# Optimization experiments

Hardware: AMD Instinct MI355X
Metric: run time of the kernel (lower is better)

Reference implementation:

```python
import jax, jax.numpy as jnp
import numpy as np

K_STEPS = 12      # number_of_prediction_steps
TEMP = 0.1        # temperature
EPS = 1e-12       # F.normalize eps


def setup_inputs() -> dict:
    key = jax.random.key(0)
    ks = jax.random.split(key, 8)
    B, T, W, D, C = 128, 512, 64, 128, 256
    g = lambda k, shape, s: (jax.random.normal(k, shape, jnp.float32) * s)
    return {
        "rr_windows": jax.random.normal(ks[0], (B, T, W), jnp.float32),
        # Encoder: Linear(window_size -> latent_dim)
        "We": g(ks[1], (W, D), 0.1), "be": jnp.zeros((D,), jnp.float32),
        # ARBlock: single-layer GRU(latent_dim -> context_dim)
        "Wi": g(ks[2], (D, 3 * C), 0.1), "Wh": g(ks[3], (C, 3 * C), 0.1),
        "bi": jnp.zeros((3 * C,), jnp.float32), "bh": jnp.zeros((3 * C,), jnp.float32),
        # Wk: K_STEPS Linears(context_dim -> latent_dim), stacked
        "Wk_w": g(ks[4], (K_STEPS, C, D), 0.1), "Wk_b": jnp.zeros((K_STEPS, D), jnp.float32),
    }


def _l2norm(x):
    n = jnp.linalg.norm(x, axis=-1, keepdims=True)
    return x / jnp.maximum(n, EPS)


def _gru(z_seq, Wi, Wh, bi, bh):
    # z_seq: [B, T, D] -> contexts [B, T, C]
    B = z_seq.shape[0]
    C = Wh.shape[0]
    x_proj = z_seq @ Wi + bi                       # [B, T, 3C] (precompute input gates)

    def step(h, x):
        hg = h @ Wh + bh
        xr, xz, xn = jnp.split(x, 3, axis=-1)
        hr, hz, hn = jnp.split(hg, 3, axis=-1)
        r = jax.nn.sigmoid(xr + hr)
        z = jax.nn.sigmoid(xz + hz)
        n = jnp.tanh(xn + r * hn)
        h_new = (1.0 - z) * n + z * h
        return h_new, h_new

    h0 = jnp.zeros((B, C), z_seq.dtype)
    _, hs = jax.lax.scan(step, h0, jnp.swapaxes(x_proj, 0, 1))  # [T, B, C]
    return jnp.swapaxes(hs, 0, 1)


def reference(rr_windows, We, be, Wi, Wh, bi, bh, Wk_w, Wk_b):
    B, T, W = rr_windows.shape
    # Encoder + normalize
    z_seq = _l2norm(rr_windows @ We + be)          # [B, T, D]
    # AR context
    c_seq = _gru(z_seq, Wi, Wh, bi, bh)            # [B, T, C]

    Tp = T - K_STEPS
    c_t = c_seq[:, :Tp, :]                         # [B, Tp, C]
    # all K predictions at once, then normalize
    pred = jnp.einsum('btc,kcd->kbtd', c_t, Wk_w) + Wk_b[:, None, None, :]
    pred = _l2norm(pred)                           # [K, B, Tp, D]
    # z_future[k, :, t] = z_seq[:, t + k + 1]
    zf = jnp.stack([jax.lax.dynamic_slice_in_dim(z_seq, k + 1, Tp, axis=1)
                    for k in range(K_STEPS)])      # [K, B, Tp, D]
    # logits[k, t, i, j] = pred[k, i, t] . z_future[k, j, t] / temp
    logits = jnp.einsum('kbtd,kctd->ktbc', pred, zf) / TEMP  # [K, Tp, B, B]

    lse = jax.nn.logsumexp(logits, axis=-1)        # [K, Tp, B]
    diag = jnp.einsum('ktbb->ktb', logits)
    avg_loss = jnp.mean(lse - diag)
    labels = jnp.arange(B)
    avg_accuracy = jnp.mean((jnp.argmax(logits, axis=-1) == labels).astype(jnp.float32)) * 100.0
    return avg_loss, avg_accuracy, z_seq, c_seq
```

## Files before the change

kernel.cpp:

```cpp
#include <hip/hip_runtime.h>
#include <math.h>

#define B_  128
#define T_  512
#define W_  64
#define D_  128
#define C_  256
#define K_  12
#define TP_ 500
#define N_SAMPLES 768000

typedef _Float16 half2v __attribute__((ext_vector_type(2)));
typedef _Float16 f16x8  __attribute__((ext_vector_type(8)));
typedef float    f32x4  __attribute__((ext_vector_type(4)));

__device__ __forceinline__ unsigned int pack2(float a, float b) {
  unsigned short ua = __builtin_bit_cast(unsigned short, (_Float16)a);
  unsigned short ub = __builtin_bit_cast(unsigned short, (_Float16)b);
  return (unsigned int)ua | ((unsigned int)ub << 16);
}

__global__ __launch_bounds__(128) void z_kernel(const float* __restrict__ rr,
                                                const float* __restrict__ We,
                                                const float* __restrict__ be,
                                                float* __restrict__ z_out,
                                                _Float16* __restrict__ z16) {
  int row = blockIdx.x;
  int d   = threadIdx.x;
  __shared__ float s_rr[64];
  __shared__ float s_red[128];
  if (d < 64) s_rr[d] = rr[row * 64 + d];
  __syncthreads();
  float acc = be[d];
#pragma unroll
  for (int w = 0; w < 64; ++w) acc = fmaf(s_rr[w], We[w * 128 + d], acc);
  s_red[d] = acc * acc;
  __syncthreads();
#pragma unroll
  for (int s = 64; s > 0; s >>= 1) {
    if (d < s) s_red[d] += s_red[d + s];
    __syncthreads();
  }
  float inv = 1.0f / fmaxf(sqrtf(s_red[0]), 1e-12f);
  float zv = acc * inv;
  z_out[row * 128 + d] = zv;
  z16[(size_t)row * 128 + d] = (_Float16)zv;
}

__global__ __launch_bounds__(256) void wiT_kernel(const float* __restrict__ Wi,
                                                  _Float16* __restrict__ wiT) {
  int id = blockIdx.x * 256 + threadIdx.x;
  int k   = id / 768;
  int col = id % 768;
  wiT[(size_t)col * 128 + k] = (_Float16)Wi[id];
}

__global__ __launch_bounds__(256, 2) void xproj_mfma(const _Float16* __restrict__ z16,
                                                     const _Float16* __restrict__ wiT,
                                                     const float* __restrict__ bi,
                                                     _Float16* __restrict__ xp) {
  int rb  = blockIdx.x * 128;
  int cb  = blockIdx.y * 128;
  int tid  = threadIdx.x;
  int wv   = tid >> 6;
  int lane = tid & 63;
  int n15  = lane & 15;
  int q    = lane >> 4;

  __shared__ __align__(16) _Float16 sA[128 * 72];
  __shared__ __align__(16) _Float16 sB[128 * 72];

  f32x4 acc[2][8];
#pragma unroll
  for (int a = 0; a < 2; ++a)
#pragma unroll
    for (int m = 0; m < 8; ++m) acc[a][m] = (f32x4){0.f, 0.f, 0.f, 0.f};

#pragma unroll
  for (int p = 0; p < 2; ++p) {
#pragma unroll
    for (int it = 0; it < 4; ++it) {
      int id = tid + it * 256;
      int r  = id >> 3;
      int c8 = (id & 7) * 8;
      *(uint4*)(&sA[r * 72 + c8]) =
          *(const uint4*)(z16 + (size_t)(rb + r) * 128 + p * 64 + c8);
      *(uint4*)(&sB[r * 72 + c8]) =
          *(const uint4*)(wiT + (size_t)(cb + r) * 128 + p * 64 + c8);
    }
    __syncthreads();
#pragma unroll
    for (int ks = 0; ks < 2; ++ks) {
      f16x8 bf[2];
#pragma unroll
      for (int ntl = 0; ntl < 2; ++ntl)
        bf[ntl] = *(const f16x8*)(&sB[((wv * 2 + ntl) * 16 + n15) * 72 + ks * 32 + q * 8]);
#pragma unroll
      for (int mt = 0; mt < 8; ++mt) {
        f16x8 af = *(const f16x8*)(&sA[(mt * 16 + n15) * 72 + ks * 32 + q * 8]);
        acc[0][mt] = __builtin_amdgcn_mfma_f32_16x16x32_f16(af, bf[0], acc[0][mt], 0, 0, 0);
        acc[1][mt] = __builtin_amdgcn_mfma_f32_16x16x32_f16(af, bf[1], acc[1][mt], 0, 0, 0);
      }
    }
    __syncthreads();
  }

#pragma unroll
  for (int ntl = 0; ntl < 2; ++ntl) {
    int col = cb + (wv * 2 + ntl) * 16 + n15;
    float bb = bi[col];
#pragma unroll
    for (int mt = 0; mt < 8; ++mt) {
#pragma unroll
      for (int r = 0; r < 4; ++r) {
        int row = rb + mt * 16 + q * 4 + r;
        xp[(size_t)row * 768 + col] = (_Float16)(acc[ntl][mt][r] + bb);
      }
    }
  }
}

__global__ __launch_bounds__(256) void whT_kernel(const float* __restrict__ Wh,
                                                  unsigned int* __restrict__ whT) {
  int g = blockIdx.x * 256 + threadIdx.x;
  int i = g / 768;
  int j = g % 768;
  float lo = Wh[(size_t)(2 * i) * 768 + j];
  float hi = Wh[(size_t)(2 * i + 1) * 768 + j];
  whT[(size_t)j * 128 + i] = pack2(lo, hi);
}

__global__ __launch_bounds__(256) void wkT_kernel(const float* __restrict__ Wk_w,
                                                  _Float16* __restrict__ wkT) {
  int id = blockIdx.x * 256 + threadIdx.x;
  int k = id >> 15;
  int rem = id & 32767;
  int c = rem >> 7;
  int d = rem & 127;
  wkT[((size_t)k * 128 + d) * 256 + c] = (_Float16)Wk_w[id];
}

__global__ __launch_bounds__(1024) void gru_kernel(const _Float16* __restrict__ xp,
                                                   const unsigned int* __restrict__ whT,
                                                   const float* __restrict__ bh,
                                                   float* __restrict__ c_out,
                                                   _Float16* __restrict__ c16) {
  __shared__ __align__(16) unsigned int s_h2[2][128];
  int tid  = threadIdx.x;
  int b    = blockIdx.x;
  int w    = tid >> 6;
  int lane = tid & 63;
  int n15  = lane & 15;
  int q    = lane >> 4;
  int ch   = w * 16 + n15;

  uint4 wf[3][8];
#pragma unroll
  for (int g = 0; g < 3; ++g) {
    const uint4* src = (const uint4*)(whT + (size_t)(g * 256 + ch) * 128);
#pragma unroll
    for (int kt = 0; kt < 8; ++kt) wf[g][kt] = src[kt * 4 + q];
  }

  if (tid < 128) s_h2[0][tid] = 0u;

  float bhr = bh[ch], bhz = bh[256 + ch], bhn = bh[512 + ch];
  const _Float16* xb = xp + (size_t)b * 512 * 768;
  float xr_n = (float)xb[ch];
  float xz_n = (float)xb[256 + ch];
  float xn_n = (float)xb[512 + ch];
  float h = 0.f;
  __syncthreads();

  for (int t = 0; t < 512; ++t) {
    const char* hb = (const char*)(&s_h2[t & 1][0]) + q * 16;
    f32x4 a0 = (f32x4){0.f, 0.f, 0.f, 0.f};
    f32x4 a1 = (f32x4){0.f, 0.f, 0.f, 0.f};
    f32x4 a2 = (f32x4){0.f, 0.f, 0.f, 0.f};
#pragma unroll
    for (int kt = 0; kt < 8; ++kt) {
      f16x8 af = *(const f16x8*)(hb + kt * 64);
      a0 = __builtin_amdgcn_mfma_f32_16x16x32_f16(af, __builtin_bit_cast(f16x8, wf[0][kt]), a0, 0, 0, 0);
      a1 = __builtin_amdgcn_mfma_f32_16x16x32_f16(af, __builtin_bit_cast(f16x8, wf[1][kt]), a1, 0, 0, 0);
      a2 = __builtin_amdgcn_mfma_f32_16x16x32_f16(af, __builtin_bit_cast(f16x8, wf[2][kt]), a2, 0, 0, 0);
    }

    float xr_c = xr_n, xz_c = xz_n, xn_c = xn_n;
    if (t < 511) {
      const _Float16* p = xb + (size_t)(t + 1) * 768;
      xr_n = (float)p[ch];
      xz_n = (float)p[256 + ch];
      xn_n = (float)p[512 + ch];
    }

    float hr = a0[0] + bhr;
    float hz = a1[0] + bhz;
    float hn = a2[0] + bhn;
    float r = __builtin_amdgcn_rcpf(1.f + __expf(-(xr_c + hr)));
    float z = __builtin_amdgcn_rcpf(1.f + __expf(-(xz_c + hz)));
    float y = xn_c + r * hn;
    y = fminf(10.f, fmaxf(-10.f, y));
    float ey = __expf(-2.f * y);
    float n = (1.f - ey) * __builtin_amdgcn_rcpf(1.f + ey);
    h = (1.f - z) * n + z * h;

    if (q == 0) {
      ((_Float16*)(&s_h2[(t & 1) ^ 1][0]))[ch] = (_Float16)h;
      c_out[((size_t)b * 512 + t) * 256 + ch] = h;
      c16[((size_t)b * 512 + t) * 256 + ch] = (_Float16)h;
    }
    __syncthreads();
  }
}

__global__ __launch_bounds__(256, 2) void cpc_kernel(const _Float16* __restrict__ z16,
                                                     const _Float16* __restrict__ c16,
                                                     const _Float16* __restrict__ wkT,
                                                     const float* __restrict__ Wk_b,
                                                     float2* __restrict__ partials) {
  int k   = blockIdx.x;
  int t   = blockIdx.y;
  int tid = threadIdx.x;
  int wv   = tid >> 6;
  int lane = tid & 63;
  int n15  = lane & 15;
  int q    = lane >> 4;

  __shared__ __align__(16) _Float16 sA[128 * 72];
  __shared__ __align__(16) _Float16 sB[128 * 72];
  __shared__ __align__(16) _Float16 sP[128 * 136];
  __shared__ float s_bias[128];

  if (tid < 128) s_bias[tid] = Wk_b[k * 128 + tid];

  f32x4 acc[2][8];
#pragma unroll
  for (int a = 0; a < 2; ++a)
#pragma unroll
    for (int m = 0; m < 8; ++m) acc[a][m] = (f32x4){0.f, 0.f, 0.f, 0.f};

  const _Float16* wk_base = wkT + (size_t)k * 128 * 256;

  for (int p = 0; p < 4; ++p) {
#pragma unroll
    for (int it = 0; it < 4; ++it) {
      int id = tid + it * 256;
      int r  = id >> 3;
      int c8 = (id & 7) * 8;
      *(uint4*)(&sA[r * 72 + c8]) =
          *(const uint4*)(wk_base + (size_t)r * 256 + p * 64 + c8);
      *(uint4*)(&sB[r * 72 + c8]) =
          *(const uint4*)(c16 + ((size_t)r * 512 + t) * 256 + p * 64 + c8);
    }
    __syncthreads();
#pragma unroll
    for (int ks = 0; ks < 2; ++ks) {
      f16x8 bf[2];
#pragma unroll
      for (int ntl = 0; ntl < 2; ++ntl)
        bf[ntl] = *(const f16x8*)(&sB[((wv * 2 + ntl) * 16 + n15) * 72 + ks * 32 + q * 8]);
#pragma unroll
      for (int mt = 0; mt < 8; ++mt) {
        f16x8 af = *(const f16x8*)(&sA[(mt * 16 + n15) * 72 + ks * 32 + q * 8]);
        acc[0][mt] = __builtin_amdgcn_mfma_f32_16x16x32_f16(af, bf[0], acc[0][mt], 0, 0, 0);
        acc[1][mt] = __builtin_amdgcn_mfma_f32_16x16x32_f16(af, bf[1], acc[1][mt], 0, 0, 0);
      }
    }
    __syncthreads();
  }

  float scale[2];
#pragma unroll
  for (int ntl = 0; ntl < 2; ++ntl) {
    float ssq = 0.f;
#pragma unroll
    for (int mt = 0; mt < 8; ++mt)
#pragma unroll
      for (int r = 0; r < 4; ++r) {
        float v = acc[ntl][mt][r] + s_bias[mt * 16 + q * 4 + r];
        acc[ntl][mt][r] = v;
        ssq = fmaf(v, v, ssq);
      }
    ssq += __shfl_xor(ssq, 16);
    ssq += __shfl_xor(ssq, 32);
    scale[ntl] = 10.0f / fmaxf(sqrtf(ssq), 1e-12f);
  }

#pragma unroll
  for (int ntl = 0; ntl < 2; ++ntl) {
    int bi = (wv * 2 + ntl) * 16 + n15;
#pragma unroll
    for (int mt = 0; mt < 8; ++mt) {
      uint2 v;
      v.x = pack2(acc[ntl][mt][0] * scale[ntl], acc[ntl][mt][1] * scale[ntl]);
      v.y = pack2(acc[ntl][mt][2] * scale[ntl], acc[ntl][mt][3] * scale[ntl]);
      *(uint2*)(&sP[bi * 136 + mt * 16 + q * 4]) = v;
    }
  }

  int tz = t + k + 1;
#pragma unroll
  for (int it = 0; it < 4; ++it) {
    int id = tid + it * 256;
    int r  = id >> 3;
    int d8 = (id & 7) * 8;
    *(uint4*)(&sA[r * 72 + d8]) =
        *(const uint4*)(z16 + ((size_t)r * 512 + tz) * 128 + d8);
    *(uint4*)(&sB[r * 72 + d8]) =
        *(const uint4*)(z16 + ((size_t)r * 512 + tz) * 128 + 64 + d8);
  }
  __syncthreads();

  f32x4 lacc[2][8];
#pragma unroll
  for (int a = 0; a < 2; ++a)
#pragma unroll
    for (int m = 0; m < 8; ++m) lacc[a][m] = (f32x4){0.f, 0.f, 0.f, 0.f};

#pragma unroll
  for (int pan = 0; pan < 2; ++pan) {
#pragma unroll
    for (int ks = 0; ks < 2; ++ks) {
      f16x8 af[2];
#pragma unroll
      for (int mtl = 0; mtl < 2; ++mtl)
        af[mtl] = *(const f16x8*)(&sP[((wv * 2 + mtl) * 16 + n15) * 136 + pan * 64 + ks * 32 + q * 8]);
#pragma unroll
      for (int nt = 0; nt < 8; ++nt) {
        f16x8 bf = pan
          ? *(const f16x8*)(&sB[(nt * 16 + n15) * 72 + ks * 32 + q * 8])
          : *(const f16x8*)(&sA[(nt * 16 + n15) * 72 + ks * 32 + q * 8]);
        lacc[0][nt] = __builtin_amdgcn_mfma_f32_16x16x32_f16(af[0], bf, lacc[0][nt], 0, 0, 0);
        lacc[1][nt] = __builtin_amdgcn_mfma_f32_16x16x32_f16(af[1], bf, lacc[1][nt], 0, 0, 0);
      }
    }
  }

  float loss_acc = 0.f, corr_acc = 0.f;
#pragma unroll
  for (int mtl = 0; mtl < 2; ++mtl) {
    int dnt = wv * 2 + mtl;
#pragma unroll
    for (int r = 0; r < 4; ++r) {
      int b = (wv * 2 + mtl) * 16 + q * 4 + r;
      float m = -1e30f; int idx = 1 << 30; float diag = 0.f;
#pragma unroll
      for (int nt = 0; nt < 8; ++nt) {
        float v = lacc[mtl][nt][r];
        int c2 = nt * 16 + n15;
        if (v > m) { m = v; idx = c2; }
        if (nt == dnt && n15 == (b & 15)) diag = v;
      }
#pragma unroll
      for (int s = 1; s <= 8; s <<= 1) {
        float om = __shfl_xor(m, s);
        int   oi = __shfl_xor(idx, s);
        if (om > m || (om == m && oi < idx)) { m = om; idx = oi; }
      }
      float e = 0.f;
#pragma unroll
      for (int nt = 0; nt < 8; ++nt) e += __expf(lacc[mtl][nt][r] - m);
#pragma unroll
      for (int s = 1; s <= 8; s <<= 1) e += __shfl_xor(e, s);
      if (n15 == (b & 15)) {
        float lse = m + __logf(e);
        loss_acc += lse - diag;
        corr_acc += (idx == b) ? 1.0f : 0.0f;
      }
    }
  }
#pragma unroll
  for (int s = 1; s <= 32; s <<= 1) {
    loss_acc += __shfl_xor(loss_acc, s);
    corr_acc += __shfl_xor(corr_acc, s);
  }

  if (lane == 0) {
    s_bias[wv * 2 + 0] = loss_acc;
    s_bias[wv * 2 + 1] = corr_acc;
  }
  __syncthreads();
  if (tid == 0) {
    float L = s_bias[0] + s_bias[2] + s_bias[4] + s_bias[6];
    float C = s_bias[1] + s_bias[3] + s_bias[5] + s_bias[7];
    partials[k * TP_ + t] = make_float2(L, C);
  }
}

__global__ __launch_bounds__(256) void reduce_kernel(const float2* __restrict__ partials,
                                                     float* __restrict__ out) {
  float l = 0.f, c = 0.f;
  for (int i = threadIdx.x; i < K_ * TP_; i += 256) {
    float2 v = partials[i];
    l += v.x; c += v.y;
  }
#pragma unroll
  for (int s = 1; s <= 32; s <<= 1) {
    l += __shfl_xor(l, s);
    c += __shfl_xor(c, s);
  }
  __shared__ float sl[4], sc[4];
  int wv = threadIdx.x >> 6;
  if ((threadIdx.x & 63) == 0) { sl[wv] = l; sc[wv] = c; }
  __syncthreads();
  if (threadIdx.x == 0) {
    float L = sl[0] + sl[1] + sl[2] + sl[3];
    float C = sc[0] + sc[1] + sc[2] + sc[3];
    out[0] = L * (float)(1.0 / (double)N_SAMPLES);
    out[1] = C * (float)(100.0 / (double)N_SAMPLES);
  }
}

extern "C" void kernel_launch(void* const* d_in, const int* in_sizes, int n_in,
                              void* d_out, int out_size, void* d_ws, size_t ws_size,
                              hipStream_t stream) {
  (void)in_sizes; (void)n_in; (void)out_size; (void)ws_size;
  const float* rr  = (const float*)d_in[0];
  const float* We  = (const float*)d_in[1];
  const float* be  = (const float*)d_in[2];
  const float* Wi  = (const float*)d_in[3];
  const float* Wh  = (const float*)d_in[4];
  const float* bi  = (const float*)d_in[5];
  const float* bh  = (const float*)d_in[6];
  const float* Wkw = (const float*)d_in[7];
  const float* Wkb = (const float*)d_in[8];

  float* out = (float*)d_out;
  float* z   = out + 2;
  float* c   = z + (size_t)B_ * T_ * D_;

  char* ws = (char*)d_ws;
  unsigned int* whT   = (unsigned int*)ws;
  _Float16*     wkT16 = (_Float16*)(ws + 393216);
  _Float16*     z16   = (_Float16*)(ws + 1179648);
  _Float16*     c16   = (_Float16*)(ws + 17956864);
  _Float16*     xp    = (_Float16*)(ws + 51511296);
  _Float16*     wiT16 = (_Float16*)(ws + 152174592);
  float2*       parts = (float2*)(ws + 51511296);

  hipMemsetAsync(d_out, 0, 2 * sizeof(float), stream);
  z_kernel<<<B_ * T_, 128, 0, stream>>>(rr, We, be, z, z16);
  wiT_kernel<<<384, 256, 0, stream>>>(Wi, wiT16);
  whT_kernel<<<384, 256, 0, stream>>>(Wh, whT);
  wkT_kernel<<<1536, 256, 0, stream>>>(Wkw, wkT16);
  xproj_mfma<<<dim3(512, 6), 256, 0, stream>>>(z16, wiT16, bi, xp);
  gru_kernel<<<B_, 1024, 0, stream>>>(xp, whT, bh, c, c16);
  cpc_kernel<<<dim3(K_, TP_), 256, 0, stream>>>(z16, c16, wkT16, Wkb, parts);
  reduce_kernel<<<1, 256, 0, stream>>>(parts, out);
}
```

Baseline: 994.7 us.

## Loop all prediction steps inside one CPC block to reuse context tile

The CPC kernel now launches one block per time step and loops over the 12 prediction heads internally. The context tile for that time step is loaded into shared memory once and reused across all heads, instead of being reloaded by 12 separate blocks. In exchange the grid shrinks from 6000 to 500 blocks. Shared memory use also rises, which forces one block per CU and may hurt occupancy and latency hiding. The reduce kernel now sums only 500 partials.

```diff
diff --git a/kernel.cpp b/kernel.cpp
--- a/kernel.cpp
+++ b/kernel.cpp
@@ -213,184 +213,196 @@
   }
 }
 
-__global__ __launch_bounds__(256, 2) void cpc_kernel(const _Float16* __restrict__ z16,
+__global__ __launch_bounds__(256, 1) void cpc_kernel(const _Float16* __restrict__ z16,
                                                      const _Float16* __restrict__ c16,
                                                      const _Float16* __restrict__ wkT,
                                                      const float* __restrict__ Wk_b,
                                                      float2* __restrict__ partials) {
-  int k   = blockIdx.x;
-  int t   = blockIdx.y;
+  int t   = blockIdx.x;
   int tid = threadIdx.x;
   int wv   = tid >> 6;
   int lane = tid & 63;
   int n15  = lane & 15;
   int q    = lane >> 4;
 
-  __shared__ __align__(16) _Float16 sA[128 * 72];
-  __shared__ __align__(16) _Float16 sB[128 * 72];
+  __shared__ __align__(16) _Float16 sCt[4][128 * 72];
+  __shared__ __align__(16) _Float16 sW[2][128 * 72];
   __shared__ __align__(16) _Float16 sP[128 * 136];
-  __shared__ float s_bias[128];
-
-  if (tid < 128) s_bias[tid] = Wk_b[k * 128 + tid];
-
-  f32x4 acc[2][8];
-#pragma unroll
-  for (int a = 0; a < 2; ++a)
-#pragma unroll
-    for (int m = 0; m < 8; ++m) acc[a][m] = (f32x4){0.f, 0.f, 0.f, 0.f};
-
-  const _Float16* wk_base = wkT + (size_t)k * 128 * 256;
-
-  for (int p = 0; p < 4; ++p) {
+  __shared__ float s_biasAll[12 * 128];
+  __shared__ float s_red[8];
+
+#pragma unroll
+  for (int it = 0; it < 16; ++it) {
+    int id  = tid + it * 256;
+    int p   = id >> 10;
+    int rem = id & 1023;
+    int r   = rem >> 3;
+    int c8  = (rem & 7) * 8;
+    *(uint4*)(&sCt[p][r * 72 + c8]) =
+        *(const uint4*)(c16 + ((size_t)r * 512 + t) * 256 + p * 64 + c8);
+  }
+  for (int i = tid; i < 12 * 128; i += 256) s_biasAll[i] = Wk_b[i];
+  __syncthreads();
+
+  float loss_acc = 0.f, corr_acc = 0.f;
+
+  for (int k = 0; k < 12; ++k) {
+    const _Float16* wk_base = wkT + (size_t)k * 128 * 256;
+
+    f32x4 acc[2][8];
+#pragma unroll
+    for (int a = 0; a < 2; ++a)
+#pragma unroll
+      for (int m = 0; m < 8; ++m) acc[a][m] = (f32x4){0.f, 0.f, 0.f, 0.f};
+
+    for (int p = 0; p < 4; ++p) {
+#pragma unroll
+      for (int it = 0; it < 4; ++it) {
+        int id = tid + it * 256;
+        int r  = id >> 3;
+        int c8 = (id & 7) * 8;
+        *(uint4*)(&sW[p & 1][r * 72 + c8]) =
+            *(const uint4*)(wk_base + (size_t)r * 256 + p * 64 + c8);
+      }
+      __syncthreads();
+#pragma unroll
+      for (int ks = 0; ks < 2; ++ks) {
+        f16x8 bf[2];
+#pragma unroll
+        for (int ntl = 0; ntl < 2; ++ntl)
+          bf[ntl] = *(const f16x8*)(&sCt[p][((wv * 2 + ntl) * 16 + n15) * 72 + ks * 32 + q * 8]);
+#pragma unroll
+        for (int mt = 0; mt < 8; ++mt) {
+          f16x8 af = *(const f16x8*)(&sW[p & 1][(mt * 16 + n15) * 72 + ks * 32 + q * 8]);
+          acc[0][mt] = __builtin_amdgcn_mfma_f32_16x16x32_f16(af, bf[0], acc[0][mt], 0, 0, 0);
+          acc[1][mt] = __builtin_amdgcn_mfma_f32_16x16x32_f16(af, bf[1], acc[1][mt], 0, 0, 0);
+        }
+      }
+      __syncthreads();
+    }
+
+    const float* s_bias = s_biasAll + k * 128;
+    float scale[2];
+#pragma unroll
+    for (int ntl = 0; ntl < 2; ++ntl) {
+      float ssq = 0.f;
+#pragma unroll
+      for (int mt = 0; mt < 8; ++mt)
+#pragma unroll
+        for (int r = 0; r < 4; ++r) {
+          float v = acc[ntl][mt][r] + s_bias[mt * 16 + q * 4 + r];
+          acc[ntl][mt][r] = v;
+          ssq = fmaf(v, v, ssq);
+        }
+      ssq += __shfl_xor(ssq, 16);
+      ssq += __shfl_xor(ssq, 32);
+      scale[ntl] = 10.0f / fmaxf(sqrtf(ssq), 1e-12f);
+    }
+
+#pragma unroll
+    for (int ntl = 0; ntl < 2; ++ntl) {
+      int bi = (wv * 2 + ntl) * 16 + n15;
+#pragma unroll
+      for (int mt = 0; mt < 8; ++mt) {
+        uint2 v;
+        v.x = pack2(acc[ntl][mt][0] * scale[ntl], acc[ntl][mt][1] * scale[ntl]);
+        v.y = pack2(acc[ntl][mt][2] * scale[ntl], acc[ntl][mt][3] * scale[ntl]);
+        *(uint2*)(&sP[bi * 136 + mt * 16 + q * 4]) = v;
+      }
+    }
+
+    int tz = t + k + 1;
 #pragma unroll
     for (int it = 0; it < 4; ++it) {
       int id = tid + it * 256;
       int r  = id >> 3;
-      int c8 = (id & 7) * 8;
-      *(uint4*)(&sA[r * 72 + c8]) =
-          *(const uint4*)(wk_base + (size_t)r * 256 + p * 64 + c8);
-      *(uint4*)(&sB[r * 72 + c8]) =
-          *(const uint4*)(c16 + ((size_t)r * 512 + t) * 256 + p * 64 + c8);
-    }
-    __syncthreads();
-#pragma unroll
-    for (int ks = 0; ks < 2; ++ks) {
-      f16x8 bf[2];
-#pragma unroll
-      for (int ntl = 0; ntl < 2; ++ntl)
-        bf[ntl] = *(const f16x8*)(&sB[((wv * 2 + ntl) * 16 + n15) * 72 + ks * 32 + q * 8]);
-#pragma unroll
-      for (int mt = 0; mt < 8; ++mt) {
-        f16x8 af = *(const f16x8*)(&sA[(mt * 16 + n15) * 72 + ks * 32 + q * 8]);
-        acc[0][mt] = __builtin_amdgcn_mfma_f32_16x16x32_f16(af, bf[0], acc[0][mt], 0, 0, 0);
-        acc[1][mt] = __builtin_amdgcn_mfma_f32_16x16x32_f16(af, bf[1], acc[1][mt], 0, 0, 0);
-      }
-    }
-    __syncthreads();
-  }
-
-  float scale[2];
-#pragma unroll
-  for (int ntl = 0; ntl < 2; ++ntl) {
-    float ssq = 0.f;
-#pragma unroll
-    for (int mt = 0; mt < 8; ++mt)
+      int d8 = (id & 7) * 8;
+      *(uint4*)(&sW[0][r * 72 + d8]) =
+          *(const uint4*)(z16 + ((size_t)r * 512 + tz) * 128 + d8);
+      *(uint4*)(&sW[1][r * 72 + d8]) =
+          *(const uint4*)(z16 + ((size_t)r * 512 + tz) * 128 + 64 + d8);
+    }
+    __syncthreads();
+
+    f32x4 lacc[2][8];
+#pragma unroll
+    for (int a = 0; a < 2; ++a)
+#pragma unroll
+      for (int m = 0; m < 8; ++m) lacc[a][m] = (f32x4){0.f, 0.f, 0.f, 0.f};
+
+#pragma unroll
+    for (int pan = 0; pan < 2; ++pan) {
+#pragma unroll
+      for (int ks = 0; ks < 2; ++ks) {
+        f16x8 af[2];
+#pragma unroll
+        for (int mtl = 0; mtl < 2; ++mtl)
+          af[mtl] = *(const f16x8*)(&sP[((wv * 2 + mtl) * 16 + n15) * 136 + pan * 64 + ks * 32 + q * 8]);
+#pragma unroll
+        for (int nt = 0; nt < 8; ++nt) {
+          f16x8 bf = *(const f16x8*)(&sW[pan][(nt * 16 + n15) * 72 + ks * 32 + q * 8]);
+          lacc[0][nt] = __builtin_amdgcn_mfma_f32_16x16x32_f16(af[0], bf, lacc[0][nt], 0, 0, 0);
+          lacc[1][nt] = __builtin_amdgcn_mfma_f32_16x16x32_f16(af[1], bf, lacc[1][nt], 0, 0, 0);
+        }
+      }
+    }
+
+#pragma unroll
+    for (int mtl = 0; mtl < 2; ++mtl) {
+      int dnt = wv * 2 + mtl;
 #pragma unroll
       for (int r = 0; r < 4; ++r) {
-        float v = acc[ntl][mt][r] + s_bias[mt * 16 + q * 4 + r];
-        acc[ntl][mt][r] = v;
-        ssq = fmaf(v, v, ssq);
-      }
-    ssq += __shfl_xor(ssq, 16);
-    ssq += __shfl_xor(ssq, 32);
-    scale[ntl] = 10.0f / fmaxf(sqrtf(ssq), 1e-12f);
-  }
-
-#pragma unroll
-  for (int ntl = 0; ntl < 2; ++ntl) {
-    int bi = (wv * 2 + ntl) * 16 + n15;
-#pragma unroll
-    for (int mt = 0; mt < 8; ++mt) {
-      uint2 v;
-      v.x = pack2(acc[ntl][mt][0] * scale[ntl], acc[ntl][mt][1] * scale[ntl]);
-      v.y = pack2(acc[ntl][mt][2] * scale[ntl], acc[ntl][mt][3] * scale[ntl]);
-      *(uint2*)(&sP[bi * 136 + mt * 16 + q * 4]) = v;
-    }
-  }
-
-  int tz = t + k + 1;
-#pragma unroll
-  for (int it = 0; it < 4; ++it) {
-    int id = tid + it * 256;
-    int r  = id >> 3;
-    int d8 = (id & 7) * 8;
-    *(uint4*)(&sA[r * 72 + d8]) =
-        *(const uint4*)(z16 + ((size_t)r * 512 + tz) * 128 + d8);
-    *(uint4*)(&sB[r * 72 + d8]) =
-        *(const uint4*)(z16 + ((size_t)r * 512 + tz) * 128 + 64 + d8);
-  }
-  __syncthreads();
-
-  f32x4 lacc[2][8];
-#pragma unroll
-  for (int a = 0; a < 2; ++a)
-#pragma unroll
-    for (int m = 0; m < 8; ++m) lacc[a][m] = (f32x4){0.f, 0.f, 0.f, 0.f};
-
-#pragma unroll
-  for (int pan = 0; pan < 2; ++pan) {
-#pragma unroll
-    for (int ks = 0; ks < 2; ++ks) {
-      f16x8 af[2];
-#pragma unroll
-      for (int mtl = 0; mtl < 2; ++mtl)
-        af[mtl] = *(const f16x8*)(&sP[((wv * 2 + mtl) * 16 + n15) * 136 + pan * 64 + ks * 32 + q * 8]);
-#pragma unroll
-      for (int nt = 0; nt < 8; ++nt) {
-        f16x8 bf = pan
-          ? *(const f16x8*)(&sB[(nt * 16 + n15) * 72 + ks * 32 + q * 8])
-          : *(const f16x8*)(&sA[(nt * 16 + n15) * 72 + ks * 32 + q * 8]);
-        lacc[0][nt] = __builtin_amdgcn_mfma_f32_16x16x32_f16(af[0], bf, lacc[0][nt], 0, 0, 0);
-        lacc[1][nt] = __builtin_amdgcn_mfma_f32_16x16x32_f16(af[1], bf, lacc[1][nt], 0, 0, 0);
-      }
-    }
-  }
-
-  float loss_acc = 0.f, corr_acc = 0.f;
-#pragma unroll
-  for (int mtl = 0; mtl < 2; ++mtl) {
-    int dnt = wv * 2 + mtl;
-#pragma unroll
-    for (int r = 0; r < 4; ++r) {
-      int b = (wv * 2 + mtl) * 16 + q * 4 + r;
-      float m = -1e30f; int idx = 1 << 30; float diag = 0.f;
-#pragma unroll
-      for (int nt = 0; nt < 8; ++nt) {
-        float v = lacc[mtl][nt][r];
-        int c2 = nt * 16 + n15;
-        if (v > m) { m = v; idx = c2; }
-        if (nt == dnt && n15 == (b & 15)) diag = v;
-      }
-#pragma unroll
-      for (int s = 1; s <= 8; s <<= 1) {
-        float om = __shfl_xor(m, s);
-        int   oi = __shfl_xor(idx, s);
-        if (om > m || (om == m && oi < idx)) { m = om; idx = oi; }
-      }
-      float e = 0.f;
-#pragma unroll
-      for (int nt = 0; nt < 8; ++nt) e += __expf(lacc[mtl][nt][r] - m);
-#pragma unroll
-      for (int s = 1; s <= 8; s <<= 1) e += __shfl_xor(e, s);
-      if (n15 == (b & 15)) {
-        float lse = m + __logf(e);
-        loss_acc += lse - diag;
-        corr_acc += (idx == b) ? 1.0f : 0.0f;
-      }
-    }
-  }
+        int b = (wv * 2 + mtl) * 16 + q * 4 + r;
+        float m = -1e30f; int idx = 1 << 30; float diag = 0.f;
+#pragma unroll
+        for (int nt = 0; nt < 8; ++nt) {
+          float v = lacc[mtl][nt][r];
+          int c2 = nt * 16 + n15;
+          if (v > m) { m = v; idx = c2; }
+          if (nt == dnt && n15 == (b & 15)) diag = v;
+        }
+#pragma unroll
+        for (int s = 1; s <= 8; s <<= 1) {
+          float om = __shfl_xor(m, s);
+          int   oi = __shfl_xor(idx, s);
+          if (om > m || (om == m && oi < idx)) { m = om; idx = oi; }
+        }
+        float e = 0.f;
+#pragma unroll
+        for (int nt = 0; nt < 8; ++nt) e += __expf(lacc[mtl][nt][r] - m);
+#pragma unroll
+        for (int s = 1; s <= 8; s <<= 1) e += __shfl_xor(e, s);
+        if (n15 == (b & 15)) {
+          float lse = m + __logf(e);
+          loss_acc += lse - diag;
+          corr_acc += (idx == b) ? 1.0f : 0.0f;
+        }
+      }
+    }
+    __syncthreads();
+  }
+
 #pragma unroll
   for (int s = 1; s <= 32; s <<= 1) {
     loss_acc += __shfl_xor(loss_acc, s);
     corr_acc += __shfl_xor(corr_acc, s);
   }
-
   if (lane == 0) {
-    s_bias[wv * 2 + 0] = loss_acc;
-    s_bias[wv * 2 + 1] = corr_acc;
+    s_red[wv * 2 + 0] = loss_acc;
+    s_red[wv * 2 + 1] = corr_acc;
   }
   __syncthreads();
   if (tid == 0) {
-    float L = s_bias[0] + s_bias[2] + s_bias[4] + s_bias[6];
-    float C = s_bias[1] + s_bias[3] + s_bias[5] + s_bias[7];
-    partials[k * TP_ + t] = make_float2(L, C);
+    float L = s_red[0] + s_red[2] + s_red[4] + s_red[6];
+    float C = s_red[1] + s_red[3] + s_red[5] + s_red[7];
+    partials[t] = make_float2(L, C);
   }
 }
 
 __global__ __launch_bounds__(256) void reduce_kernel(const float2* __restrict__ partials,
                                                      float* __restrict__ out) {
   float l = 0.f, c = 0.f;
-  for (int i = threadIdx.x; i < K_ * TP_; i += 256) {
+  for (int i = threadIdx.x; i < TP_; i += 256) {
     float2 v = partials[i];
     l += v.x; c += v.y;
   }
@@ -445,6 +457,6 @@
   wkT_kernel<<<1536, 256, 0, stream>>>(Wkw, wkT16);
   xproj_mfma<<<dim3(512, 6), 256, 0, stream>>>(z16, wiT16, bi, xp);
   gru_kernel<<<B_, 1024, 0, stream>>>(xp, whT, bh, c, c16);
-  cpc_kernel<<<dim3(K_, TP_), 256, 0, stream>>>(z16, c16, wkT16, Wkb, parts);
+  cpc_kernel<<<TP_, 256, 0, stream>>>(z16, c16, wkT16, Wkb, parts);
   reduce_kernel<<<1, 256, 0, stream>>>(parts, out);
 }
```

Result: slower. 1.096 ms (+10.2%).
